# Performance work log

Hardware: AMD Instinct MI355X
Metric: run time of the kernel (lower is better)

## Reference

```python
import jax, jax.numpy as jnp
import numpy as np

B, NC, H, W = 8, 3, 24, 150
P = 2                      # patch size along time == sub_seq
WS = W // P                # 75 time segments per joint
N = H * WS                 # 1800 patches
PD = P * NC                # 6 time values per patch (time_values_per_joint)
D = 512                    # encoder_dim
L = 4                      # transformer depth
NH = 8
DH = D // NH
MLP = 4 * D
MASK_RATIO = 0.5
NM = int(MASK_RATIO * N)   # 900 masked patches


def setup_inputs() -> dict:
    key = jax.random.key(0)
    ks = jax.random.split(key, 20)
    s = 0.02
    img = jax.random.normal(ks[0], (B, NC, H, W), jnp.float32)
    valid_length = jax.random.randint(ks[1], (B,), 1, 151)
    # masked_indices = topk indices of uniform noise (matches torch.rand().topk)
    noise = jax.random.uniform(ks[2], (B, N), jnp.float32)
    masked_indices = jax.lax.top_k(noise, NM)[1]
    n = jax.random.normal
    return {
        "img": img,
        "pos_table": n(ks[3], (N + 1, D), jnp.float32) * s,
        "val_table": n(ks[4], (2, D), jnp.float32) * s,
        "patch_W": n(ks[5], (PD, D), jnp.float32) * s,
        "patch_b": jnp.zeros((D,), jnp.float32),
        "mask_token": n(ks[6], (D,), jnp.float32),
        "ln1_s": jnp.ones((L, D), jnp.float32),
        "ln1_b": jnp.zeros((L, D), jnp.float32),
        "Wqkv": n(ks[7], (L, D, 3 * D), jnp.float32) * s,
        "bqkv": jnp.zeros((L, 3 * D), jnp.float32),
        "Wo": n(ks[8], (L, D, D), jnp.float32) * s,
        "bo": jnp.zeros((L, D), jnp.float32),
        "ln2_s": jnp.ones((L, D), jnp.float32),
        "ln2_b": jnp.zeros((L, D), jnp.float32),
        "W1": n(ks[9], (L, D, MLP), jnp.float32) * s,
        "b1": jnp.zeros((L, MLP), jnp.float32),
        "W2": n(ks[10], (L, MLP, D), jnp.float32) * s,
        "b2": jnp.zeros((L, D), jnp.float32),
        "Wt": n(ks[11], (D, PD), jnp.float32) * s,
        "bt": jnp.zeros((PD,), jnp.float32),
        "valid_length": valid_length,
        "masked_indices": masked_indices,
    }


def _ln(x, s, b):
    m = jnp.mean(x, -1, keepdims=True)
    v = jnp.mean((x - m) ** 2, -1, keepdims=True)
    return (x - m) / jnp.sqrt(v + 1e-5) * s + b


def reference(img, pos_table, val_table, patch_W, patch_b, mask_token,
              ln1_s, ln1_b, Wqkv, bqkv, Wo, bo, ln2_s, ln2_b,
              W1, b1, W2, b2, Wt, bt, valid_length, masked_indices):
    # to_patch: [B,NC,H,W] -> [B, H*(W//P), P*NC]  (joint-major, time-segment inner)
    patches = jnp.transpose(img, (0, 2, 3, 1)).reshape(B, H, WS, PD).reshape(B, N, PD)

    # valid_segment construction (vectorized over batch)
    vl = jnp.where(valid_length == 150, 149, valid_length)
    n_valid = jnp.ceil(vl.astype(jnp.float32) / P).astype(jnp.int32)  # ceil(i/sub_seq)
    seg_t = (jnp.arange(WS)[None, :] < n_valid[:, None]).astype(jnp.int32)  # [B,WS]
    seg = jnp.concatenate([jnp.ones((B, 1), jnp.int32), jnp.tile(seg_t, (1, H))], axis=1)  # [B,N+1]

    pos_emb = (pos_table[None, :, :] + val_table[seg])[:, 1:]          # [B,N,D]
    tokens = patches @ patch_W + patch_b + pos_emb
    mask_toks = mask_token[None, None, :] + pos_emb

    br = jnp.arange(B)[:, None]
    bool_mask = jnp.zeros((B, N), bool).at[br, masked_indices].set(True)
    x = jnp.where(bool_mask[..., None], mask_toks, tokens)

    scale = 1.0 / np.sqrt(DH).astype(np.float32)
    for l in range(L):
        h = _ln(x, ln1_s[l], ln1_b[l])
        qkv = h @ Wqkv[l] + bqkv[l]
        q, k, v = [t.reshape(B, N, NH, DH) for t in jnp.split(qkv, 3, axis=-1)]
        att = jax.nn.softmax(jnp.einsum('bqhd,bkhd->bhqk', q, k) * scale, axis=-1)
        o = jnp.einsum('bhqk,bkhd->bqhd', att, v).reshape(B, N, D)
        x = x + o @ Wo[l] + bo[l]
        h = _ln(x, ln2_s[l], ln2_b[l])
        x = x + jax.nn.gelu(h @ W1[l] + b1[l]) @ W2[l] + b2[l]

    enc_masked = x[br, masked_indices]            # [B,NM,D]
    pred = enc_masked @ Wt + bt                   # [B,NM,PD]
    masked_patches = patches[br, masked_indices]  # [B,NM,PD]
    recon_loss = jnp.mean(jnp.abs(pred - masked_patches)) / NM
    return recon_loss
```

## Files before the change

kernel.cpp:

```cpp
#include <hip/hip_runtime.h>
#include <hip/hip_fp8.h>
#include <cstdint>

typedef _Float16 f16;
typedef _Float16 f16x2 __attribute__((ext_vector_type(2)));
typedef _Float16 f16x4 __attribute__((ext_vector_type(4)));
typedef _Float16 f16x8 __attribute__((ext_vector_type(8)));
typedef float    f32x4 __attribute__((ext_vector_type(4)));
typedef __hip_fp8_e4m3 fp8;
typedef long     i64;
typedef unsigned char u8;

#define BATCH 8
#define NSEQ  1800
#define DIM   512
#define NMASK 900
#define MROWS 14400

__device__ __forceinline__ void stage16(const void* g, void* lds_wave_base, int lane) {
#if __has_builtin(__builtin_amdgcn_global_load_lds)
  (void)lane;
  __builtin_amdgcn_global_load_lds((const __attribute__((address_space(1))) void*)g,
                                   (__attribute__((address_space(3))) void*)lds_wave_base,
                                   16, 0, 0);
#else
  ((uint4*)lds_wave_base)[lane] = *(const uint4*)g;
#endif
}

__device__ __forceinline__ float gelu_f(float x) {
  float x3 = x * x * x;
  float y  = 0.7978845608028654f * (x + 0.044715f * x3);
  float t;
  if (y > 15.f)       t = 1.f;
  else if (y < -15.f) t = -1.f;
  else { float e = __expf(2.f * y); t = (e - 1.f) / (e + 1.f); }
  return 0.5f * x * (1.f + t);
}

__global__ void scatter_mask(const int* __restrict__ mi, int* __restrict__ maskf) {
  int i = blockIdx.x * 256 + threadIdx.x;
  if (i < BATCH * NMASK) {
    int b = i / NMASK;
    maskf[b * NSEQ + mi[i]] = 1;
  }
}

__global__ void transposeW(const float* __restrict__ in, fp8* __restrict__ out, int K, int N) {
  long off = (long)blockIdx.z * K * N;
  const float* ip = in + off;
  fp8* op = out + off;
  __shared__ float tile[32][33];
  int n0 = blockIdx.x * 32, k0 = blockIdx.y * 32;
  int tx = threadIdx.x, ty = threadIdx.y;
#pragma unroll
  for (int i = 0; i < 4; ++i)
    tile[ty + 8 * i][tx] = ip[(long)(k0 + ty + 8 * i) * N + n0 + tx];
  __syncthreads();
#pragma unroll
  for (int i = 0; i < 4; ++i)
    op[(long)(n0 + ty + 8 * i) * K + k0 + tx] = fp8(tile[tx][ty + 8 * i]);
}

__global__ __launch_bounds__(256)
void prep_kernel(const float* __restrict__ img, const float* __restrict__ pos_table,
                 const float* __restrict__ val_table, const float* __restrict__ patch_W,
                 const float* __restrict__ patch_b, const float* __restrict__ mask_tok,
                 const int* __restrict__ valid_len, const int* __restrict__ maskf,
                 float* __restrict__ patches, f16* __restrict__ x0) {
  int n = blockIdx.x;
  int b = blockIdx.y;
  int t = threadIdx.x;
  __shared__ float p[6];
  int h = n / 75, ws = n % 75;
  if (t < 6) {
    int pp = t / 3, c = t % 3;
    float v = img[((b * 3 + c) * 24 + h) * 150 + ws * 2 + pp];
    p[t] = v;
    patches[((long)b * NSEQ + n) * 6 + t] = v;
  }
  __syncthreads();
  int vl = valid_len[b];
  if (vl == 150) vl = 149;
  int nv = (vl + 1) >> 1;
  int seg = (ws < nv) ? 1 : 0;
  bool masked = maskf[b * NSEQ + n] != 0;
  for (int d = t; d < DIM; d += 256) {
    float pos = pos_table[(long)(n + 1) * DIM + d] + val_table[seg * DIM + d];
    float v;
    if (masked) {
      v = mask_tok[d] + pos;
    } else {
      float acc = patch_b[d] + pos;
#pragma unroll
      for (int j = 0; j < 6; ++j) acc += p[j] * patch_W[j * DIM + d];
      v = acc;
    }
    x0[((long)b * NSEQ + n) * DIM + d] = (f16)v;
  }
}

__global__ __launch_bounds__(256)
void ln_kernel(const f16* __restrict__ x, const float* __restrict__ s,
               const float* __restrict__ bb, fp8* __restrict__ out) {
  const int t = threadIdx.x;
  const int wave = t >> 6, lane = t & 63;
  const int col = lane * 8;
  float sv[8], bv[8];
  {
    float4 s0 = *(const float4*)&s[col], s1 = *(const float4*)&s[col + 4];
    float4 b0 = *(const float4*)&bb[col], b1 = *(const float4*)&bb[col + 4];
    sv[0] = s0.x; sv[1] = s0.y; sv[2] = s0.z; sv[3] = s0.w;
    sv[4] = s1.x; sv[5] = s1.y; sv[6] = s1.z; sv[7] = s1.w;
    bv[0] = b0.x; bv[1] = b0.y; bv[2] = b0.z; bv[3] = b0.w;
    bv[4] = b1.x; bv[5] = b1.y; bv[6] = b1.z; bv[7] = b1.w;
  }
  long rowBase = (long)blockIdx.x * 8 + wave * 2;
#pragma unroll
  for (int rr = 0; rr < 2; ++rr) {
    long row = rowBase + rr;
    f16x8 v = *(const f16x8*)(x + row * DIM + col);
    float f[8], sum = 0.f, sq = 0.f;
#pragma unroll
    for (int j = 0; j < 8; ++j) { f[j] = (float)v[j]; sum += f[j]; sq += f[j] * f[j]; }
#pragma unroll
    for (int mk = 1; mk < 64; mk <<= 1) {
      sum += __shfl_xor(sum, mk);
      sq  += __shfl_xor(sq, mk);
    }
    float mean = sum * (1.f / DIM);
    float var  = sq * (1.f / DIM) - mean * mean;
    float rstd = rsqrtf(var + 1e-5f);
    fp8 o8[8];
#pragma unroll
    for (int j = 0; j < 8; ++j) o8[j] = fp8((f[j] - mean) * rstd * sv[j] + bv[j]);
    *(uint2*)&out[row * DIM + col] = *(const uint2*)o8;
  }
}

template <int EPI>
__global__ __launch_bounds__(256)
void gemm8_kernel(const u8* __restrict__ A, const u8* __restrict__ Bt,
                  const float* __restrict__ bias, const f16* __restrict__ res,
                  f16* __restrict__ outH, fp8* __restrict__ out8, f16* __restrict__ outV,
                  int M, int N, int K, int gx) {
  __shared__ u8 As[8 * 128 * 16];
  __shared__ u8 Bs[8 * 128 * 16];
  const int tid  = threadIdx.x;
  const int wave = tid >> 6, lane = tid & 63;
  const int quad = lane >> 4, l16 = lane & 15;
  const int wm = wave >> 1, wn = wave & 1;

  const int nwg = (int)gridDim.x;
  const int q = nwg >> 3, rr = nwg & 7;
  const int xcd = (int)blockIdx.x & 7, idx = (int)blockIdx.x >> 3;
  const int wg = (xcd < rr ? xcd * (q + 1) : rr * (q + 1) + (xcd - rr) * q) + idx;
  const long rowBase = (long)(wg / gx) * 128;
  const long colBase = (long)(wg % gx) * 128;

  f32x4 acc[4][4];
  f32x4 zero = {0.f, 0.f, 0.f, 0.f};
#pragma unroll
  for (int ni = 0; ni < 4; ++ni)
#pragma unroll
    for (int mi = 0; mi < 4; ++mi) acc[ni][mi] = zero;

  long rA0 = rowBase + lane;       if (rA0 > M - 1) rA0 = M - 1;
  long rA1 = rowBase + 64 + lane;  if (rA1 > M - 1) rA1 = M - 1;
  const u8* Arow0 = A + rA0 * K + wave * 16;
  const u8* Arow1 = A + rA1 * K + wave * 16;
  const u8* Brow0 = Bt + (colBase + lane) * K + wave * 16;
  const u8* Brow1 = Bt + (colBase + 64 + lane) * K + wave * 16;
  u8* AsC0 = As + wave * 2048;
  u8* AsC1 = AsC0 + 64 * 16;
  u8* AsC2 = As + (wave + 4) * 2048;
  u8* AsC3 = AsC2 + 64 * 16;
  u8* BsC0 = Bs + wave * 2048;
  u8* BsC1 = BsC0 + 64 * 16;
  u8* BsC2 = Bs + (wave + 4) * 2048;
  u8* BsC3 = BsC2 + 64 * 16;

  for (int kt = 0; kt < K; kt += 128) {
    __syncthreads();
    stage16(Arow0 + kt,      AsC0, lane);
    stage16(Arow1 + kt,      AsC1, lane);
    stage16(Arow0 + kt + 64, AsC2, lane);
    stage16(Arow1 + kt + 64, AsC3, lane);
    stage16(Brow0 + kt,      BsC0, lane);
    stage16(Brow1 + kt,      BsC1, lane);
    stage16(Brow0 + kt + 64, BsC2, lane);
    stage16(Brow1 + kt + 64, BsC3, lane);
    __syncthreads();
#pragma unroll
    for (int ks = 0; ks < 4; ++ks) {
      const int cb = (2 * ks + (quad >> 1)) * 2048 + (quad & 1) * 8;
      i64 af[4], bf[4];
#pragma unroll
      for (int mi = 0; mi < 4; ++mi)
        af[mi] = *(const i64*)&As[cb + (wm * 64 + mi * 16 + l16) * 16];
#pragma unroll
      for (int ni = 0; ni < 4; ++ni)
        bf[ni] = *(const i64*)&Bs[cb + (wn * 64 + ni * 16 + l16) * 16];
#pragma unroll
      for (int ni = 0; ni < 4; ++ni)
#pragma unroll
        for (int mi = 0; mi < 4; ++mi)
          acc[ni][mi] = __builtin_amdgcn_mfma_f32_16x16x32_fp8_fp8(bf[ni], af[mi], acc[ni][mi], 0, 0, 0);
    }
  }

  if (EPI == 0 && outV != nullptr && colBase >= 1024) {
    const int hh = (int)((colBase - 1024) >> 6) + wn;
#pragma unroll
    for (int mi = 0; mi < 4; ++mi) {
      long m = rowBase + wm * 64 + mi * 16 + l16;
      if (m < M) {
        int b = (int)m / NSEQ;
        int key = (int)m - b * NSEQ;
        f16* vdst = outV + ((long)(b * 8 + hh) * 64) * NSEQ + key;
#pragma unroll
        for (int ni = 0; ni < 4; ++ni) {
          long n = colBase + wn * 64 + ni * 16 + quad * 4;
          float4 bv = *(const float4*)&bias[n];
          f32x4 v = acc[ni][mi];
#pragma unroll
          for (int r = 0; r < 4; ++r)
            vdst[(long)(ni * 16 + quad * 4 + r) * NSEQ] = (f16)(v[r] + (&bv.x)[r]);
        }
      }
    }
    return;
  }

#pragma unroll
  for (int mi = 0; mi < 4; ++mi) {
    long m = rowBase + wm * 64 + mi * 16 + l16;
    if (m < M) {
#pragma unroll
      for (int ni = 0; ni < 4; ++ni) {
        long n = colBase + wn * 64 + ni * 16 + quad * 4;
        float4 bv = *(const float4*)&bias[n];
        f32x4 v = acc[ni][mi];
        v[0] += bv.x; v[1] += bv.y; v[2] += bv.z; v[3] += bv.w;
        long o = m * N + n;
        if (EPI == 1) {
          f16x4 rr4 = *(const f16x4*)&res[o];
          f16x4 ov;
#pragma unroll
          for (int r = 0; r < 4; ++r) ov[r] = (f16)(v[r] + (float)rr4[r]);
          *(f16x4*)&outH[o] = ov;
        } else if (EPI == 2) {
          fp8 hv[4];
#pragma unroll
          for (int r = 0; r < 4; ++r) hv[r] = fp8(gelu_f(v[r]));
          *(uint32_t*)&out8[o] = *(const uint32_t*)hv;
        } else {
          f16x4 hv;
#pragma unroll
          for (int r = 0; r < 4; ++r) hv[r] = (f16)v[r];
          *(f16x4*)&outH[o] = hv;
        }
      }
    }
  }
}

#define ATTN_TILE_BODY(MASKV)                                                           \
  {                                                                                     \
    _Pragma("unroll")                                                                   \
    for (int n = 0; n < 4; ++n) {                                                       \
      f16x8 b0 = *(const f16x8*)&Ks[n * 16 + l16][quad * 8];                            \
      f16x8 b1 = *(const f16x8*)&Ks[n * 16 + l16][32 + quad * 8];                       \
      f32x4 zz = {0.f, 0.f, 0.f, 0.f};                                                  \
      zz = __builtin_amdgcn_mfma_f32_16x16x32_f16(qfA0, b0, zz, 0, 0, 0);               \
      zz = __builtin_amdgcn_mfma_f32_16x16x32_f16(qfA1, b1, zz, 0, 0, 0);               \
      bool bad = (MASKV) && (n > 0 || l16 >= 8);                                        \
      _Pragma("unroll")                                                                 \
      for (int r = 0; r < 4; ++r) {                                                     \
        float pp = exp2f(fmaf(zz[r], K1, -8.f));                                        \
        if (bad) pp = 0.f;                                                              \
        Ps[wave * 16 + quad * 4 + r][n * 16 + l16] = (f16)pp;                           \
        lsA[r] += pp;                                                                   \
      }                                                                                 \
    }                                                                                   \
    {                                                                                   \
      f16x8 pa0 = *(const f16x8*)&Ps[wave * 16 + l16][quad * 8];                        \
      f16x8 pa1 = *(const f16x8*)&Ps[wave * 16 + l16][32 + quad * 8];                   \
      _Pragma("unroll")                                                                 \
      for (int nt = 0; nt < 4; ++nt) {                                                  \
        f16x8 vb0 = *(const f16x8*)&Vs[nt * 16 + l16][quad * 8];                        \
        f16x8 vb1 = *(const f16x8*)&Vs[nt * 16 + l16][32 + quad * 8];                   \
        oA[nt] = __builtin_amdgcn_mfma_f32_16x16x32_f16(pa0, vb0, oA[nt], 0, 0, 0);     \
        oA[nt] = __builtin_amdgcn_mfma_f32_16x16x32_f16(pa1, vb1, oA[nt], 0, 0, 0);     \
      }                                                                                 \
    }                                                                                   \
    _Pragma("unroll")                                                                   \
    for (int n = 0; n < 4; ++n) {                                                       \
      f16x8 b0 = *(const f16x8*)&Ks[n * 16 + l16][quad * 8];                            \
      f16x8 b1 = *(const f16x8*)&Ks[n * 16 + l16][32 + quad * 8];                       \
      f32x4 zz = {0.f, 0.f, 0.f, 0.f};                                                  \
      zz = __builtin_amdgcn_mfma_f32_16x16x32_f16(qfB0, b0, zz, 0, 0, 0);               \
      zz = __builtin_amdgcn_mfma_f32_16x16x32_f16(qfB1, b1, zz, 0, 0, 0);               \
      bool bad = (MASKV) && (n > 0 || l16 >= 8);                                        \
      _Pragma("unroll")                                                                 \
      for (int r = 0; r < 4; ++r) {                                                     \
        float pp = exp2f(fmaf(zz[r], K1, -8.f));                                        \
        if (bad) pp = 0.f;                                                              \
        Ps[wave * 16 + quad * 4 + r][n * 16 + l16] = (f16)pp;                           \
        lsB[r] += pp;                                                                   \
      }                                                                                 \
    }                                                                                   \
    {                                                                                   \
      f16x8 pa0 = *(const f16x8*)&Ps[wave * 16 + l16][quad * 8];                        \
      f16x8 pa1 = *(const f16x8*)&Ps[wave * 16 + l16][32 + quad * 8];                   \
      _Pragma("unroll")                                                                 \
      for (int nt = 0; nt < 4; ++nt) {                                                  \
        f16x8 vb0 = *(const f16x8*)&Vs[nt * 16 + l16][quad * 8];                        \
        f16x8 vb1 = *(const f16x8*)&Vs[nt * 16 + l16][32 + quad * 8];                   \
        oB[nt] = __builtin_amdgcn_mfma_f32_16x16x32_f16(pa0, vb0, oB[nt], 0, 0, 0);     \
        oB[nt] = __builtin_amdgcn_mfma_f32_16x16x32_f16(pa1, vb1, oB[nt], 0, 0, 0);     \
      }                                                                                 \
    }                                                                                   \
  }

__global__ __launch_bounds__(256, 4)
void attn_kernel(const f16* __restrict__ qkv, const f16* __restrict__ Vt,
                 fp8* __restrict__ out) {
  const int g = blockIdx.x;
  const int hi = g / 120, rem = g % 120;
  const int qt = rem >> 3;
  const int bh = hi * 8 + (rem & 7);
  const int b = bh >> 3, hh = bh & 7;
  const int t = threadIdx.x;
  const int wave = t >> 6, lane = t & 63;
  const int quad = lane >> 4, l16 = lane & 15;
  const int q0 = qt * 128;
  const long baseBN = (long)b * NSEQ;
  const float K1 = 0.18033688011112042f;

  __shared__ f16 Ks[64][80];
  __shared__ f16 Vs[64][80];
  __shared__ f16 Ps[64][80];

  int qrA = q0 + wave * 32 + l16;      if (qrA > NSEQ - 1) qrA = NSEQ - 1;
  int qrB = q0 + wave * 32 + 16 + l16; if (qrB > NSEQ - 1) qrB = NSEQ - 1;
  const f16* QpA = qkv + (baseBN + qrA) * 1536 + hh * 64 + quad * 8;
  const f16* QpB = qkv + (baseBN + qrB) * 1536 + hh * 64 + quad * 8;
  f16x8 qfA0 = *(const f16x8*)(QpA);
  f16x8 qfA1 = *(const f16x8*)(QpA + 32);
  f16x8 qfB0 = *(const f16x8*)(QpB);
  f16x8 qfB1 = *(const f16x8*)(QpB + 32);

  f32x4 oA[4], oB[4];
  float lsA[4] = {0.f, 0.f, 0.f, 0.f}, lsB[4] = {0.f, 0.f, 0.f, 0.f};
#pragma unroll
  for (int nt = 0; nt < 4; ++nt) { oA[nt] = f32x4{0,0,0,0}; oB[nt] = f32x4{0,0,0,0}; }

  const f16* Kg = qkv + baseBN * 1536 + hh * 64 + 512;
  const f16* Vg = Vt + (long)bh * 64 * 1800;
  const int sr = t >> 3, sc = t & 7;
  const uint4 z4 = {0u, 0u, 0u, 0u};

  const f16* KgS = Kg + (long)sr * 1536 + sc * 8;
  const f16* VgS = Vg + (long)sr * 1800 + sc * 8;

  uint4 pk0 = *(const uint4*)(KgS);
  uint4 pk1 = *(const uint4*)(KgS + (long)32 * 1536);
  uint4 pv0 = *(const uint4*)(VgS);
  uint4 pv1 = *(const uint4*)(VgS + (long)32 * 1800);

  for (int kt = 0; kt < 28; ++kt) {
    __syncthreads();
    *(uint4*)&Ks[sr][sc * 8]      = pk0;
    *(uint4*)&Ks[sr + 32][sc * 8] = pk1;
    *(uint4*)&Vs[sr][sc * 8]      = pv0;
    *(uint4*)&Vs[sr + 32][sc * 8] = pv1;
    {
      long ko = (long)(kt + 1) * 64;
      pk0 = *(const uint4*)(KgS + ko * 1536);
      pk1 = *(const uint4*)(KgS + (ko + 32) * 1536);
      bool vok = (ko + sc * 8) < NSEQ;
      pv0 = vok ? *(const uint4*)(VgS + ko) : z4;
      pv1 = vok ? *(const uint4*)(VgS + (long)32 * 1800 + ko) : z4;
    }
    __syncthreads();
    ATTN_TILE_BODY(false)
  }
  {
    __syncthreads();
    *(uint4*)&Ks[sr][sc * 8]      = pk0;
    *(uint4*)&Ks[sr + 32][sc * 8] = pk1;
    *(uint4*)&Vs[sr][sc * 8]      = pv0;
    *(uint4*)&Vs[sr + 32][sc * 8] = pv1;
    __syncthreads();
    ATTN_TILE_BODY(true)
  }

#pragma unroll
  for (int mk = 1; mk < 16; mk <<= 1)
#pragma unroll
    for (int r = 0; r < 4; ++r) {
      lsA[r] += __shfl_xor(lsA[r], mk);
      lsB[r] += __shfl_xor(lsB[r], mk);
    }

#pragma unroll
  for (int r = 0; r < 4; ++r) {
    int qgA = q0 + wave * 32 + quad * 4 + r;
    if (qgA < NSEQ) {
      float inv = 1.f / lsA[r];
#pragma unroll
      for (int nt = 0; nt < 4; ++nt)
        out[(baseBN + qgA) * 512 + hh * 64 + nt * 16 + l16] = fp8(oA[nt][r] * inv);
    }
    int qgB = qgA + 16;
    if (qgB < NSEQ) {
      float inv = 1.f / lsB[r];
#pragma unroll
      for (int nt = 0; nt < 4; ++nt)
        out[(baseBN + qgB) * 512 + hh * 64 + nt * 16 + l16] = fp8(oB[nt][r] * inv);
    }
  }
}

__global__ __launch_bounds__(192)
void head_kernel(const f16* __restrict__ x, const float* __restrict__ patches,
                 const int* __restrict__ mi, const float* __restrict__ Wt,
                 const float* __restrict__ bt, float* __restrict__ lossAcc) {
  int t = threadIdx.x;
  int pd = t / 32, sg = t % 32;
  float wt[16];
#pragma unroll
  for (int k = 0; k < 16; ++k) wt[k] = Wt[(sg * 16 + k) * 6 + pd];
  float btv = bt[pd];
  float accAll = 0.f;
  for (int rr = 0; rr < 32; ++rr) {
    int bi = blockIdx.x * 32 + rr;
    int b = bi / NMASK;
    int idx = mi[bi];
    const f16x8* xr8 = (const f16x8*)(x + ((long)b * NSEQ + idx) * DIM);
    float acc = 0.f;
#pragma unroll
    for (int j = 0; j < 2; ++j) {
      f16x8 xa = xr8[sg * 2 + j];
#pragma unroll
      for (int k2 = 0; k2 < 8; ++k2) acc += (float)xa[k2] * wt[j * 8 + k2];
    }
#pragma unroll
    for (int mk = 1; mk < 32; mk <<= 1) acc += __shfl_xor(acc, mk);
    if (sg == 0) {
      float pred = acc + btv;
      accAll += fabsf(pred - patches[((long)b * NSEQ + idx) * 6 + pd]);
    }
  }
  if (sg == 0) atomicAdd(lossAcc, accAll);
}

__global__ void finalize_kernel(const float* __restrict__ acc, float* __restrict__ out) {
  if (threadIdx.x == 0 && blockIdx.x == 0)
    out[0] = acc[0] * (1.0f / 38880000.0f);
}

extern "C" void kernel_launch(void* const* d_in, const int* in_sizes, int n_in,
                              void* d_out, int out_size, void* d_ws, size_t ws_size,
                              hipStream_t stream) {
  (void)in_sizes; (void)n_in; (void)out_size; (void)ws_size;
  const float* img       = (const float*)d_in[0];
  const float* pos_table = (const float*)d_in[1];
  const float* val_table = (const float*)d_in[2];
  const float* patch_W   = (const float*)d_in[3];
  const float* patch_b   = (const float*)d_in[4];
  const float* mask_tok  = (const float*)d_in[5];
  const float* ln1_s     = (const float*)d_in[6];
  const float* ln1_b     = (const float*)d_in[7];
  const float* Wqkv      = (const float*)d_in[8];
  const float* bqkv      = (const float*)d_in[9];
  const float* Wo        = (const float*)d_in[10];
  const float* bo        = (const float*)d_in[11];
  const float* ln2_s     = (const float*)d_in[12];
  const float* ln2_b     = (const float*)d_in[13];
  const float* W1        = (const float*)d_in[14];
  const float* b1        = (const float*)d_in[15];
  const float* W2        = (const float*)d_in[16];
  const float* b2        = (const float*)d_in[17];
  const float* Wt        = (const float*)d_in[18];
  const float* bt        = (const float*)d_in[19];
  const int* valid_len   = (const int*)d_in[20];
  const int* mask_idx    = (const int*)d_in[21];

  char* p = (char*)d_ws;
  auto alloc = [&](size_t bytes) { char* r = p; p += (bytes + 511) & ~(size_t)511; return r; };
  float* patches = (float*)alloc((size_t)MROWS * 6 * 4);
  int*   maskf   = (int*)alloc((size_t)MROWS * 4);
  float* lossAcc = (float*)alloc(256);
  f16*   x       = (f16*)alloc((size_t)MROWS * 512 * 2);
  fp8*   h       = (fp8*)alloc((size_t)MROWS * 512 + 512);
  f16*   Vt      = (f16*)alloc((size_t)64 * 64 * 1800 * 2 + 512);
  f16*   qkv     = (f16*)alloc((size_t)MROWS * 2048 * 2);
  fp8*   attn    = (fp8*)alloc((size_t)MROWS * 512);
  fp8*   WqT     = (fp8*)alloc((size_t)4 * 1536 * 512);
  fp8*   WoT     = (fp8*)alloc((size_t)4 * 512 * 512);
  fp8*   W1T     = (fp8*)alloc((size_t)4 * 2048 * 512);
  fp8*   W2T     = (fp8*)alloc((size_t)4 * 512 * 2048);
  fp8*   hid     = (fp8*)qkv;

  hipMemsetAsync(maskf, 0, (size_t)MROWS * 4, stream);
  hipMemsetAsync(lossAcc, 0, 4, stream);
  scatter_mask<<<29, 256, 0, stream>>>(mask_idx, maskf);

  transposeW<<<dim3(48, 16, 4), dim3(32, 8), 0, stream>>>(Wqkv, WqT, 512, 1536);
  transposeW<<<dim3(16, 16, 4), dim3(32, 8), 0, stream>>>(Wo,  WoT, 512, 512);
  transposeW<<<dim3(64, 16, 4), dim3(32, 8), 0, stream>>>(W1,  W1T, 512, 2048);
  transposeW<<<dim3(16, 64, 4), dim3(32, 8), 0, stream>>>(W2,  W2T, 2048, 512);

  prep_kernel<<<dim3(1800, 8), 256, 0, stream>>>(img, pos_table, val_table, patch_W, patch_b,
                                                 mask_tok, valid_len, maskf, patches, x);

  for (int l = 0; l < 4; ++l) {
    ln_kernel<<<1800, 256, 0, stream>>>(x, ln1_s + l * 512, ln1_b + l * 512, h);
    gemm8_kernel<0><<<dim3(12 * 113), 256, 0, stream>>>((const u8*)h, (const u8*)(WqT + (size_t)l * 1536 * 512),
                                                        bqkv + l * 1536, nullptr, qkv, nullptr, Vt,
                                                        MROWS, 1536, 512, 12);
    attn_kernel<<<dim3(960), 256, 0, stream>>>(qkv, Vt, attn);
    gemm8_kernel<1><<<dim3(4 * 113), 256, 0, stream>>>((const u8*)attn, (const u8*)(WoT + (size_t)l * 512 * 512),
                                                       bo + l * 512, x, x, nullptr, nullptr,
                                                       MROWS, 512, 512, 4);
    ln_kernel<<<1800, 256, 0, stream>>>(x, ln2_s + l * 512, ln2_b + l * 512, h);
    gemm8_kernel<2><<<dim3(16 * 113), 256, 0, stream>>>((const u8*)h, (const u8*)(W1T + (size_t)l * 2048 * 512),
                                                        b1 + l * 2048, nullptr, nullptr, hid, nullptr,
                                                        MROWS, 2048, 512, 16);
    gemm8_kernel<1><<<dim3(4 * 113), 256, 0, stream>>>((const u8*)hid, (const u8*)(W2T + (size_t)l * 512 * 2048),
                                                       b2 + l * 512, x, x, nullptr, nullptr,
                                                       MROWS, 512, 2048, 4);
  }

  head_kernel<<<225, 192, 0, stream>>>(x, patches, mask_idx, Wt, bt, lossAcc);
  finalize_kernel<<<1, 64, 0, stream>>>(lossAcc, (float*)d_out);
}
```

Measured before the change: 1.396 ms.

## Compute last layer's post-attention work only for masked rows via gathered GEMMs

In the final layer, only the masked tokens feed the loss, so the Wo projection, second layernorm and MLP are now run on the 7200 gathered masked rows instead of all 14400. A row-index table is built in the mask scatter kernel and used by the GEMM to gather A rows and residual rows, with results written into a compact buffer that the head kernel reads directly. This halves the MLP and output-projection work of the last layer at the cost of indirect row loads.

```diff
diff --git a/kernel.cpp b/kernel.cpp
--- a/kernel.cpp
+++ b/kernel.cpp
@@ -16,6 +16,7 @@
 #define DIM   512
 #define NMASK 900
 #define MROWS 14400
+#define MMASK 7200
 
 __device__ __forceinline__ void stage16(const void* g, void* lds_wave_base, int lane) {
 #if __has_builtin(__builtin_amdgcn_global_load_lds)
@@ -38,11 +39,14 @@
   return 0.5f * x * (1.f + t);
 }
 
-__global__ void scatter_mask(const int* __restrict__ mi, int* __restrict__ maskf) {
+__global__ void scatter_mask(const int* __restrict__ mi, int* __restrict__ maskf,
+                             int* __restrict__ grows) {
   int i = blockIdx.x * 256 + threadIdx.x;
   if (i < BATCH * NMASK) {
     int b = i / NMASK;
-    maskf[b * NSEQ + mi[i]] = 1;
+    int row = b * NSEQ + mi[i];
+    maskf[row] = 1;
+    grows[i] = row;
   }
 }
 
@@ -143,6 +147,7 @@
 void gemm8_kernel(const u8* __restrict__ A, const u8* __restrict__ Bt,
                   const float* __restrict__ bias, const f16* __restrict__ res,
                   f16* __restrict__ outH, fp8* __restrict__ out8, f16* __restrict__ outV,
+                  const int* __restrict__ gidx,
                   int M, int N, int K, int gx) {
   __shared__ u8 As[8 * 128 * 16];
   __shared__ u8 Bs[8 * 128 * 16];
@@ -167,6 +172,7 @@
 
   long rA0 = rowBase + lane;       if (rA0 > M - 1) rA0 = M - 1;
   long rA1 = rowBase + 64 + lane;  if (rA1 > M - 1) rA1 = M - 1;
+  if (gidx) { rA0 = gidx[rA0]; rA1 = gidx[rA1]; }
   const u8* Arow0 = A + rA0 * K + wave * 16;
   const u8* Arow1 = A + rA1 * K + wave * 16;
   const u8* Brow0 = Bt + (colBase + lane) * K + wave * 16;
@@ -236,6 +242,7 @@
   for (int mi = 0; mi < 4; ++mi) {
     long m = rowBase + wm * 64 + mi * 16 + l16;
     if (m < M) {
+      long gm = gidx ? (long)gidx[m] : m;
 #pragma unroll
       for (int ni = 0; ni < 4; ++ni) {
         long n = colBase + wn * 64 + ni * 16 + quad * 4;
@@ -244,7 +251,7 @@
         v[0] += bv.x; v[1] += bv.y; v[2] += bv.z; v[3] += bv.w;
         long o = m * N + n;
         if (EPI == 1) {
-          f16x4 rr4 = *(const f16x4*)&res[o];
+          f16x4 rr4 = *(const f16x4*)&res[gm * N + n];
           f16x4 ov;
 #pragma unroll
           for (int r = 0; r < 4; ++r) ov[r] = (f16)(v[r] + (float)rr4[r]);
@@ -424,7 +431,7 @@
 }
 
 __global__ __launch_bounds__(192)
-void head_kernel(const f16* __restrict__ x, const float* __restrict__ patches,
+void head_kernel(const f16* __restrict__ xm, const float* __restrict__ patches,
                  const int* __restrict__ mi, const float* __restrict__ Wt,
                  const float* __restrict__ bt, float* __restrict__ lossAcc) {
   int t = threadIdx.x;
@@ -438,7 +445,7 @@
     int bi = blockIdx.x * 32 + rr;
     int b = bi / NMASK;
     int idx = mi[bi];
-    const f16x8* xr8 = (const f16x8*)(x + ((long)b * NSEQ + idx) * DIM);
+    const f16x8* xr8 = (const f16x8*)(xm + (long)bi * DIM);
     float acc = 0.f;
 #pragma unroll
     for (int j = 0; j < 2; ++j) {
@@ -492,8 +499,10 @@
   auto alloc = [&](size_t bytes) { char* r = p; p += (bytes + 511) & ~(size_t)511; return r; };
   float* patches = (float*)alloc((size_t)MROWS * 6 * 4);
   int*   maskf   = (int*)alloc((size_t)MROWS * 4);
+  int*   grows   = (int*)alloc((size_t)MMASK * 4);
   float* lossAcc = (float*)alloc(256);
   f16*   x       = (f16*)alloc((size_t)MROWS * 512 * 2);
+  f16*   xm      = (f16*)alloc((size_t)(MMASK + 128) * 512 * 2);
   fp8*   h       = (fp8*)alloc((size_t)MROWS * 512 + 512);
   f16*   Vt      = (f16*)alloc((size_t)64 * 64 * 1800 * 2 + 512);
   f16*   qkv     = (f16*)alloc((size_t)MROWS * 2048 * 2);
@@ -506,7 +515,7 @@
 
   hipMemsetAsync(maskf, 0, (size_t)MROWS * 4, stream);
   hipMemsetAsync(lossAcc, 0, 4, stream);
-  scatter_mask<<<29, 256, 0, stream>>>(mask_idx, maskf);
+  scatter_mask<<<29, 256, 0, stream>>>(mask_idx, maskf, grows);
 
   transposeW<<<dim3(48, 16, 4), dim3(32, 8), 0, stream>>>(Wqkv, WqT, 512, 1536);
   transposeW<<<dim3(16, 16, 4), dim3(32, 8), 0, stream>>>(Wo,  WoT, 512, 512);
@@ -519,21 +528,34 @@
   for (int l = 0; l < 4; ++l) {
     ln_kernel<<<1800, 256, 0, stream>>>(x, ln1_s + l * 512, ln1_b + l * 512, h);
     gemm8_kernel<0><<<dim3(12 * 113), 256, 0, stream>>>((const u8*)h, (const u8*)(WqT + (size_t)l * 1536 * 512),
-                                                        bqkv + l * 1536, nullptr, qkv, nullptr, Vt,
+                                                        bqkv + l * 1536, nullptr, qkv, nullptr, Vt, nullptr,
                                                         MROWS, 1536, 512, 12);
     attn_kernel<<<dim3(960), 256, 0, stream>>>(qkv, Vt, attn);
-    gemm8_kernel<1><<<dim3(4 * 113), 256, 0, stream>>>((const u8*)attn, (const u8*)(WoT + (size_t)l * 512 * 512),
-                                                       bo + l * 512, x, x, nullptr, nullptr,
-                                                       MROWS, 512, 512, 4);
-    ln_kernel<<<1800, 256, 0, stream>>>(x, ln2_s + l * 512, ln2_b + l * 512, h);
-    gemm8_kernel<2><<<dim3(16 * 113), 256, 0, stream>>>((const u8*)h, (const u8*)(W1T + (size_t)l * 2048 * 512),
-                                                        b1 + l * 2048, nullptr, nullptr, hid, nullptr,
-                                                        MROWS, 2048, 512, 16);
-    gemm8_kernel<1><<<dim3(4 * 113), 256, 0, stream>>>((const u8*)hid, (const u8*)(W2T + (size_t)l * 512 * 2048),
-                                                       b2 + l * 512, x, x, nullptr, nullptr,
-                                                       MROWS, 512, 2048, 4);
-  }
-
-  head_kernel<<<225, 192, 0, stream>>>(x, patches, mask_idx, Wt, bt, lossAcc);
+    if (l < 3) {
+      gemm8_kernel<1><<<dim3(4 * 113), 256, 0, stream>>>((const u8*)attn, (const u8*)(WoT + (size_t)l * 512 * 512),
+                                                         bo + l * 512, x, x, nullptr, nullptr, nullptr,
+                                                         MROWS, 512, 512, 4);
+      ln_kernel<<<1800, 256, 0, stream>>>(x, ln2_s + l * 512, ln2_b + l * 512, h);
+      gemm8_kernel<2><<<dim3(16 * 113), 256, 0, stream>>>((const u8*)h, (const u8*)(W1T + (size_t)l * 2048 * 512),
+                                                          b1 + l * 2048, nullptr, nullptr, hid, nullptr, nullptr,
+                                                          MROWS, 2048, 512, 16);
+      gemm8_kernel<1><<<dim3(4 * 113), 256, 0, stream>>>((const u8*)hid, (const u8*)(W2T + (size_t)l * 512 * 2048),
+                                                         b2 + l * 512, x, x, nullptr, nullptr, nullptr,
+                                                         MROWS, 512, 2048, 4);
+    } else {
+      gemm8_kernel<1><<<dim3(4 * 57), 256, 0, stream>>>((const u8*)attn, (const u8*)(WoT + (size_t)l * 512 * 512),
+                                                        bo + l * 512, x, xm, nullptr, nullptr, grows,
+                                                        MMASK, 512, 512, 4);
+      ln_kernel<<<900, 256, 0, stream>>>(xm, ln2_s + l * 512, ln2_b + l * 512, h);
+      gemm8_kernel<2><<<dim3(16 * 57), 256, 0, stream>>>((const u8*)h, (const u8*)(W1T + (size_t)l * 2048 * 512),
+                                                         b1 + l * 2048, nullptr, nullptr, hid, nullptr, nullptr,
+                                                         MMASK, 2048, 512, 16);
+      gemm8_kernel<1><<<dim3(4 * 57), 256, 0, stream>>>((const u8*)hid, (const u8*)(W2T + (size_t)l * 512 * 2048),
+                                                        b2 + l * 512, xm, xm, nullptr, nullptr, nullptr,
+                                                        MMASK, 512, 2048, 4);
+    }
+  }
+
+  head_kernel<<<225, 192, 0, stream>>>(xm, patches, mask_idx, Wt, bt, lossAcc);
   finalize_kernel<<<1, 64, 0, stream>>>(lossAcc, (float*)d_out);
 }
```

Result: no change. 1.370 ms (-1.9%).
